# Performance work log

Hardware: AMD Instinct MI355X
Metric: run time of the kernel (lower is better)

## Reference

```python
import jax, jax.numpy as jnp
import numpy as np

B, T, D = 2, 2048, 1024
F = 4096
E = 8


def setup_inputs() -> dict:
    key = jax.random.key(0)
    k0, k1, k2, k3 = jax.random.split(key, 4)
    x = jax.random.normal(k0, (B, T, D), dtype=jnp.float32)
    Wg = jax.random.normal(k1, (E, D), dtype=jnp.float32) * 0.02   # gate Linear weight [E, D]
    W1 = jax.random.normal(k2, (E, D, F), dtype=jnp.float32) * 0.02  # expert up-proj
    W2 = jax.random.normal(k3, (E, F, D), dtype=jnp.float32) * 0.02  # expert down-proj
    return {"x": x, "Wg": Wg, "W1": W1, "W2": W2}


def reference(x, Wg, W1, W2):
    b, t, d = x.shape
    h = x.reshape(-1, d)                              # [N, D], N = b*t
    # --- top-2 gate ---
    logits = h @ Wg.T                                 # [N, E]
    scores, idx = jax.lax.top_k(logits, 2)            # [N, 2], [N, 2]
    scores = jax.nn.softmax(scores.astype(jnp.float32), axis=-1).astype(x.dtype)
    # --- all-expert dense FFN (SiLU MLP) ---
    up = jnp.einsum('nd,edf->enf', h, W1)             # [E, N, F]
    act = jax.nn.silu(up)
    out = jnp.einsum('enf,efd->ned', act, W2)         # [N, E, D]
    # --- combine top-2 ---
    sel = jnp.take_along_axis(out, idx[:, :, None], axis=1)  # [N, 2, D]
    y = jnp.sum(scores[:, :, None] * sel, axis=1)     # [N, D]
    return y.reshape(b, t, d)
```

## Files before the change

### kernel.cpp

```cpp
#include <hip/hip_runtime.h>
#include <hip/hip_bf16.h>
#include <stdint.h>

#define N_TOK 4096
#define D_DIM 1024
#define F_DIM 4096
#define E_NUM 8

typedef unsigned short u16;
typedef __attribute__((ext_vector_type(8))) short short8;
typedef __attribute__((ext_vector_type(4))) float f32x4;

__device__ __forceinline__ u16 f2bf(float f) {
  union { float f; uint32_t u; } v; v.f = f;
  uint32_t u = v.u;
  uint32_t r = (u + 0x7FFFu + ((u >> 16) & 1u)) >> 16;
  return (u16)r;
}

__device__ __forceinline__ void gld_lds16(const u16* g, u16* l) {
  __builtin_amdgcn_global_load_lds(
      (const __attribute__((address_space(1))) uint32_t*)g,
      (__attribute__((address_space(3))) uint32_t*)l, 16, 0, 0);
}

__global__ __launch_bounds__(256) void transpose_cvt_kernel(
    const float* __restrict__ in, u16* __restrict__ out, int R, int C) {
  __shared__ u16 tile[64][72];
  int e = blockIdx.z;
  int r0 = blockIdx.y * 64, c0 = blockIdx.x * 64;
  const float* src = in + (size_t)e * R * C;
  u16* dst = out + (size_t)e * R * C;
  int tid = threadIdx.x;
  int lr = tid & 15;
  int rr = tid >> 4;
#pragma unroll
  for (int p = 0; p < 4; ++p) {
    int r = rr + p * 16;
    float4 v = *(const float4*)&src[(size_t)(r0 + r) * C + c0 + lr * 4];
    tile[lr * 4 + 0][r] = f2bf(v.x);
    tile[lr * 4 + 1][r] = f2bf(v.y);
    tile[lr * 4 + 2][r] = f2bf(v.z);
    tile[lr * 4 + 3][r] = f2bf(v.w);
  }
  __syncthreads();
#pragma unroll
  for (int p = 0; p < 4; ++p) {
    int c = rr + p * 16;
    ushort4 o = *(const ushort4*)&tile[c][lr * 4];
    *(ushort4*)&dst[(size_t)(c0 + c) * R + r0 + lr * 4] = o;
  }
}

__global__ void gate_kernel(const float* __restrict__ x, const float* __restrict__ Wg,
                            u16* __restrict__ xb, int2* __restrict__ choice,
                            float* __restrict__ sc2) {
  int n = blockIdx.x;
  int l = threadIdx.x;
  const float* xr = x + (size_t)n * D_DIM;
  u16* xbr = xb + (size_t)n * D_DIM;
  float acc[E_NUM];
#pragma unroll
  for (int e = 0; e < E_NUM; ++e) acc[e] = 0.f;
  for (int d = l; d < D_DIM; d += 64) {
    float xv = xr[d];
    xbr[d] = f2bf(xv);
#pragma unroll
    for (int e = 0; e < E_NUM; ++e) acc[e] += xv * Wg[e * D_DIM + d];
  }
#pragma unroll
  for (int e = 0; e < E_NUM; ++e) {
    float v = acc[e];
#pragma unroll
    for (int off = 32; off > 0; off >>= 1) v += __shfl_xor(v, off);
    acc[e] = v;
  }
  if (l == 0) {
    int i0 = 0; float m0 = acc[0];
#pragma unroll
    for (int e = 1; e < E_NUM; ++e) if (acc[e] > m0) { m0 = acc[e]; i0 = e; }
    int i1 = -1; float m1 = -INFINITY;
#pragma unroll
    for (int e = 0; e < E_NUM; ++e) if (e != i0 && acc[e] > m1) { m1 = acc[e]; i1 = e; }
    float z = __expf(m1 - m0);
    float s0 = 1.f / (1.f + z);
    sc2[n * 2 + 0] = s0;
    sc2[n * 2 + 1] = 1.f - s0;
    choice[n] = make_int2(i0, i1);
  }
}

__global__ void route_kernel(const int2* __restrict__ choice, int* __restrict__ cnt,
                             int* __restrict__ tok_list) {
  int e = blockIdx.x;
  int l = threadIdx.x;
  unsigned long long below = (l == 0) ? 0ull : ((~0ull) >> (64 - l));
  int c = 0;
  for (int it = 0; it < N_TOK / 64; ++it) {
    int n = it * 64 + l;
    int2 ch = choice[n];
    unsigned long long b0 = __ballot(ch.x == e);
    if (ch.x == e) tok_list[e * N_TOK + c + __popcll(b0 & below)] = 2 * n;
    c += __popcll(b0);
    unsigned long long b1 = __ballot(ch.y == e);
    if (ch.y == e) tok_list[e * N_TOK + c + __popcll(b1 & below)] = 2 * n + 1;
    c += __popcll(b1);
  }
  if (l == 0) cnt[e] = c;
}

__global__ void prefix_kernel(const int* __restrict__ cnt, int* __restrict__ base) {
  if (threadIdx.x == 0) {
    int s = 0;
    for (int e = 0; e < E_NUM; ++e) { base[e] = s; s += cnt[e]; }
  }
}


__global__ __launch_bounds__(256) void up_gemm(
    const u16* __restrict__ xb, const u16* __restrict__ w1t,
    const int* __restrict__ cnt, const int* __restrict__ base,
    const int* __restrict__ tok_list, u16* __restrict__ act) {
  __shared__ u16 As[128 * 32];
  __shared__ u16 Bs[128 * 32];

  const int bid = blockIdx.x;
  const int orig = (bid & 7) * 1024 + (bid >> 3);
  const int bx = orig & 31, by = (orig >> 5) & 31, e = orig >> 10;

  const int ce = cnt[e];
  const int row0 = by * 128;
  if (row0 >= ce) return;
  const int col0 = bx * 128;
  const int be = base[e];

  const int tid = threadIdx.x;
  const int wave = tid >> 6, lane = tid & 63;
  const int wm = wave >> 1, wn = wave & 1;
  const int lr = lane & 15, kq = lane >> 4;

  const int rs0 = wave * 32 + (lane >> 2);
  const int rs1 = rs0 + 16;
  const int kb = (((lane & 3) ^ ((lane >> 3) & 3)) * 8);
  const int kq8 = ((kq ^ ((lr >> 1) & 3)) * 8);

  int ga0 = row0 + rs0, ga1 = row0 + rs1;
  int e0 = (ga0 < ce) ? (tok_list[e * N_TOK + ga0] & (2 * N_TOK - 1)) : 0;
  int e1 = (ga1 < ce) ? (tok_list[e * N_TOK + ga1] & (2 * N_TOK - 1)) : 0;
  const u16* srcA0 = xb + (e0 >> 1) * D_DIM + kb;
  const u16* srcA1 = xb + (e1 >> 1) * D_DIM + kb;
  const u16* srcB0 = w1t + (size_t)(e * F_DIM + col0 + rs0) * D_DIM + kb;
  const u16* srcB1 = w1t + (size_t)(e * F_DIM + col0 + rs1) * D_DIM + kb;
  u16* ldsA0 = As + (wave * 2 + 0) * 512;
  u16* ldsA1 = As + (wave * 2 + 1) * 512;
  u16* ldsB0 = Bs + (wave * 2 + 0) * 512;
  u16* ldsB1 = Bs + (wave * 2 + 1) * 512;

  f32x4 acc[4][4];
#pragma unroll
  for (int m = 0; m < 4; ++m)
#pragma unroll
    for (int n = 0; n < 4; ++n) acc[m][n] = (f32x4){0.f, 0.f, 0.f, 0.f};

  for (int k0 = 0; k0 < D_DIM; k0 += 32) {
    gld_lds16(srcA0 + k0, ldsA0);
    gld_lds16(srcA1 + k0, ldsA1);
    gld_lds16(srcB0 + k0, ldsB0);
    gld_lds16(srcB1 + k0, ldsB1);
    __syncthreads();
    short8 a[4], b[4];
#pragma unroll
    for (int m = 0; m < 4; ++m)
      a[m] = *(const short8*)&As[(wm * 64 + m * 16 + lr) * 32 + kq8];
#pragma unroll
    for (int n = 0; n < 4; ++n)
      b[n] = *(const short8*)&Bs[(wn * 64 + n * 16 + lr) * 32 + kq8];
#pragma unroll
    for (int m = 0; m < 4; ++m)
#pragma unroll
      for (int n = 0; n < 4; ++n)
        acc[m][n] = __builtin_amdgcn_mfma_f32_16x16x32_bf16(a[m], b[n], acc[m][n], 0, 0, 0);
    __syncthreads();
  }

#pragma unroll
  for (int m = 0; m < 4; ++m) {
#pragma unroll
    for (int rg = 0; rg < 4; ++rg) {
      int row = wm * 64 + m * 16 + kq * 4 + rg;
      int i = row0 + row;
      if (i < ce) {
        u16* dst = act + (size_t)(be + i) * F_DIM + col0 + wn * 64;
#pragma unroll
        for (int n = 0; n < 4; ++n) {
          float v = acc[m][n][rg];
          float s = v / (1.f + __expf(-v));
          dst[n * 16 + lr] = f2bf(s);
        }
      }
    }
  }
}

__global__ __launch_bounds__(512) void down_gemm(
    const u16* __restrict__ act, const u16* __restrict__ w2t,
    const int* __restrict__ cnt, const int* __restrict__ base,
    const int* __restrict__ tok_list, const float* __restrict__ sc2,
    float* __restrict__ out) {
  __shared__ u16 As[2][128 * 32];
  __shared__ u16 Bs[2][128 * 32];
  __shared__ int toks[128];

  const int bid = blockIdx.x;
  const int orig = (bid & 7) * 256 + (bid >> 3);
  const int bx = orig & 7, by = (orig >> 3) & 31, e = orig >> 8;

  const int ce = cnt[e];
  const int row0 = by * 128;
  if (row0 >= ce) return;
  const int col0 = bx * 128;
  const int be = base[e];

  const int tid = threadIdx.x;
  const int wave = tid >> 6, lane = tid & 63;
  const int wm = wave >> 2, wn = wave & 3;
  const int lr = lane & 15, kq = lane >> 4;

  if (tid < 128) {
    int i = row0 + tid;
    toks[tid] = (i < ce) ? tok_list[e * N_TOK + i] : -1;
  }
  __syncthreads();

  const int rsA = wave * 16 + (lane >> 2);
  const int kb = (((lane & 3) ^ ((lane >> 3) & 3)) * 8);
  const int kq8 = ((kq ^ ((lr >> 1) & 3)) * 8);

  int ra = min(be + row0 + rsA, 2 * N_TOK - 1);
  const u16* srcA = act + (size_t)ra * F_DIM + kb;
  const u16* srcB = w2t + (size_t)(e * D_DIM + col0 + rsA) * F_DIM + kb;

  f32x4 acc[4][2];
#pragma unroll
  for (int m = 0; m < 4; ++m)
#pragma unroll
    for (int n = 0; n < 2; ++n) acc[m][n] = (f32x4){0.f, 0.f, 0.f, 0.f};

#define DSTAGE(k0, b)                              \
  do {                                             \
    gld_lds16(srcA + (k0), &As[b][wave * 512]);    \
    gld_lds16(srcB + (k0), &Bs[b][wave * 512]);    \
  } while (0)

#define DCOMPUTE(b)                                                           \
  do {                                                                        \
    short8 a[4], bb[2];                                                       \
    _Pragma("unroll") for (int m = 0; m < 4; ++m)                             \
        a[m] = *(const short8*)&As[b][(wm * 64 + m * 16 + lr) * 32 + kq8];    \
    _Pragma("unroll") for (int n = 0; n < 2; ++n)                             \
        bb[n] = *(const short8*)&Bs[b][(wn * 32 + n * 16 + lr) * 32 + kq8];   \
    _Pragma("unroll") for (int m = 0; m < 4; ++m)                             \
        _Pragma("unroll") for (int n = 0; n < 2; ++n)                         \
            acc[m][n] = __builtin_amdgcn_mfma_f32_16x16x32_bf16(a[m], bb[n], acc[m][n], 0, 0, 0); \
  } while (0)

  const int NT = F_DIM / 32;
  DSTAGE(0, 0);
  DSTAGE(32, 1);
  asm volatile("s_waitcnt vmcnt(2)" ::: "memory");
  __builtin_amdgcn_s_barrier();
  __builtin_amdgcn_sched_barrier(0);
  int cur = 0;
  for (int t = 0; t < NT; ++t) {
    DCOMPUTE(cur);
    __builtin_amdgcn_sched_barrier(0);
    __builtin_amdgcn_s_barrier();
    __builtin_amdgcn_sched_barrier(0);
    if (t + 2 < NT) {
      DSTAGE((t + 2) * 32, cur);
      asm volatile("s_waitcnt vmcnt(2)" ::: "memory");
    } else {
      asm volatile("s_waitcnt vmcnt(0)" ::: "memory");
    }
    __builtin_amdgcn_s_barrier();
    __builtin_amdgcn_sched_barrier(0);
    cur ^= 1;
  }
#undef DSTAGE
#undef DCOMPUTE

#pragma unroll
  for (int m = 0; m < 4; ++m) {
#pragma unroll
    for (int rg = 0; rg < 4; ++rg) {
      int row = wm * 64 + m * 16 + kq * 4 + rg;
      int ent = toks[row];
      if (ent >= 0) {
        int tokn = ent >> 1;
        float sc = sc2[tokn * 2 + (ent & 1)];
        float* dst = out + (size_t)tokn * D_DIM + col0 + wn * 32;
#pragma unroll
        for (int n = 0; n < 2; ++n)
          atomicAdd(&dst[n * 16 + lr], acc[m][n][rg] * sc);
      }
    }
  }
}

extern "C" void kernel_launch(void* const* d_in, const int* in_sizes, int n_in,
                              void* d_out, int out_size, void* d_ws, size_t ws_size,
                              hipStream_t stream) {
  const float* x  = (const float*)d_in[0];
  const float* Wg = (const float*)d_in[1];
  const float* W1 = (const float*)d_in[2];
  const float* W2 = (const float*)d_in[3];
  float* out = (float*)d_out;

  char* ws = (char*)d_ws;
  size_t off = 0;
  u16* xb  = (u16*)(ws + off); off += (size_t)N_TOK * D_DIM * 2;
  u16* w1t = (u16*)(ws + off); off += (size_t)E_NUM * F_DIM * D_DIM * 2;
  u16* w2t = (u16*)(ws + off); off += (size_t)E_NUM * D_DIM * F_DIM * 2;
  u16* act = (u16*)(ws + off); off += (size_t)2 * N_TOK * F_DIM * 2;
  int* tok_list = (int*)(ws + off); off += (size_t)E_NUM * N_TOK * 4;
  float* sc2 = (float*)(ws + off); off += (size_t)N_TOK * 2 * 4;
  int2* choice = (int2*)(ws + off); off += (size_t)N_TOK * 8;
  int* cnt  = (int*)(ws + off); off += 128;
  int* base = (int*)(ws + off); off += 128;

  hipMemsetAsync(d_out, 0, (size_t)out_size * 4, stream);

  {
    dim3 blk(256, 1, 1);
    dim3 g1(F_DIM / 64, D_DIM / 64, E_NUM);
    transpose_cvt_kernel<<<g1, blk, 0, stream>>>(W1, w1t, D_DIM, F_DIM);
    dim3 g2(D_DIM / 64, F_DIM / 64, E_NUM);
    transpose_cvt_kernel<<<g2, blk, 0, stream>>>(W2, w2t, F_DIM, D_DIM);
  }

  gate_kernel<<<N_TOK, 64, 0, stream>>>(x, Wg, xb, choice, sc2);
  route_kernel<<<E_NUM, 64, 0, stream>>>(choice, cnt, tok_list);
  prefix_kernel<<<1, 1, 0, stream>>>(cnt, base);

  up_gemm<<<dim3(8192), 256, 0, stream>>>(xb, w1t, cnt, base, tok_list, act);
  down_gemm<<<dim3(2048), 512, 0, stream>>>(act, w2t, cnt, base, tok_list, sc2, out);
}
```

Baseline: 327.2 us.

## Enlarge down-proj GEMM tile to 256x128 with K=64 stages

```diff
diff --git a/kernel.cpp b/kernel.cpp
--- a/kernel.cpp
+++ b/kernel.cpp
@@ -116,7 +116,6 @@
   }
 }
 
-
 __global__ __launch_bounds__(256) void up_gemm(
     const u16* __restrict__ xb, const u16* __restrict__ w1t,
     const int* __restrict__ cnt, const int* __restrict__ base,
@@ -207,67 +206,81 @@
     const int* __restrict__ cnt, const int* __restrict__ base,
     const int* __restrict__ tok_list, const float* __restrict__ sc2,
     float* __restrict__ out) {
-  __shared__ u16 As[2][128 * 32];
-  __shared__ u16 Bs[2][128 * 32];
-  __shared__ int toks[128];
+  __shared__ u16 As[2][256 * 64];
+  __shared__ u16 Bs[2][128 * 64];
+  __shared__ int toks[256];
 
   const int bid = blockIdx.x;
-  const int orig = (bid & 7) * 256 + (bid >> 3);
-  const int bx = orig & 7, by = (orig >> 3) & 31, e = orig >> 8;
+  const int orig = (bid & 7) * 128 + (bid >> 3);
+  const int bx = orig & 7, by = (orig >> 3) & 15, e = orig >> 7;
 
   const int ce = cnt[e];
-  const int row0 = by * 128;
+  const int row0 = by * 256;
   if (row0 >= ce) return;
   const int col0 = bx * 128;
   const int be = base[e];
 
   const int tid = threadIdx.x;
   const int wave = tid >> 6, lane = tid & 63;
-  const int wm = wave >> 2, wn = wave & 3;
+  const int wm = wave >> 1, wn = wave & 1;
   const int lr = lane & 15, kq = lane >> 4;
 
-  if (tid < 128) {
+  if (tid < 256) {
     int i = row0 + tid;
     toks[tid] = (i < ce) ? tok_list[e * N_TOK + i] : -1;
   }
   __syncthreads();
 
-  const int rsA = wave * 16 + (lane >> 2);
-  const int kb = (((lane & 3) ^ ((lane >> 3) & 3)) * 8);
-  const int kq8 = ((kq ^ ((lr >> 1) & 3)) * 8);
-
-  int ra = min(be + row0 + rsA, 2 * N_TOK - 1);
-  const u16* srcA = act + (size_t)ra * F_DIM + kb;
-  const u16* srcB = w2t + (size_t)(e * D_DIM + col0 + rsA) * F_DIM + kb;
-
-  f32x4 acc[4][2];
+  const int srow = lane >> 3;
+  const int kb = ((lane & 7) ^ srow) * 8;
+  const int rsw = (lr & 7);
+
+  const u16* srcA[4];
+#pragma unroll
+  for (int j = 0; j < 4; ++j) {
+    int ra = min(be + row0 + wave * 32 + j * 8 + srow, 2 * N_TOK - 1);
+    srcA[j] = act + (size_t)ra * F_DIM + kb;
+  }
+  const u16* srcB[2];
+#pragma unroll
+  for (int j = 0; j < 2; ++j) {
+    int rb = e * D_DIM + col0 + wave * 16 + j * 8 + srow;
+    srcB[j] = w2t + (size_t)rb * F_DIM + kb;
+  }
+
+  f32x4 acc[4][4];
 #pragma unroll
   for (int m = 0; m < 4; ++m)
 #pragma unroll
-    for (int n = 0; n < 2; ++n) acc[m][n] = (f32x4){0.f, 0.f, 0.f, 0.f};
-
-#define DSTAGE(k0, b)                              \
-  do {                                             \
-    gld_lds16(srcA + (k0), &As[b][wave * 512]);    \
-    gld_lds16(srcB + (k0), &Bs[b][wave * 512]);    \
+    for (int n = 0; n < 4; ++n) acc[m][n] = (f32x4){0.f, 0.f, 0.f, 0.f};
+
+#define DSTAGE(k0, b)                                              \
+  do {                                                             \
+    _Pragma("unroll") for (int j = 0; j < 4; ++j)                  \
+        gld_lds16(srcA[j] + (k0), &As[b][(wave * 4 + j) * 512]);   \
+    _Pragma("unroll") for (int j = 0; j < 2; ++j)                  \
+        gld_lds16(srcB[j] + (k0), &Bs[b][(wave * 2 + j) * 512]);   \
   } while (0)
 
-#define DCOMPUTE(b)                                                           \
-  do {                                                                        \
-    short8 a[4], bb[2];                                                       \
-    _Pragma("unroll") for (int m = 0; m < 4; ++m)                             \
-        a[m] = *(const short8*)&As[b][(wm * 64 + m * 16 + lr) * 32 + kq8];    \
-    _Pragma("unroll") for (int n = 0; n < 2; ++n)                             \
-        bb[n] = *(const short8*)&Bs[b][(wn * 32 + n * 16 + lr) * 32 + kq8];   \
-    _Pragma("unroll") for (int m = 0; m < 4; ++m)                             \
-        _Pragma("unroll") for (int n = 0; n < 2; ++n)                         \
-            acc[m][n] = __builtin_amdgcn_mfma_f32_16x16x32_bf16(a[m], bb[n], acc[m][n], 0, 0, 0); \
+#define DCOMPUTE(b)                                                             \
+  do {                                                                          \
+    _Pragma("unroll") for (int kk = 0; kk < 2; ++kk) {                          \
+      const int ks = ((kk * 4 + kq) ^ rsw) * 8;                                 \
+      short8 a[4], bb[4];                                                       \
+      _Pragma("unroll") for (int m = 0; m < 4; ++m)                             \
+          a[m] = *(const short8*)&As[b][(wm * 64 + m * 16 + lr) * 64 + ks];     \
+      _Pragma("unroll") for (int n = 0; n < 4; ++n)                             \
+          bb[n] = *(const short8*)&Bs[b][(wn * 64 + n * 16 + lr) * 64 + ks];    \
+      _Pragma("unroll") for (int m = 0; m < 4; ++m)                             \
+          _Pragma("unroll") for (int n = 0; n < 4; ++n)                         \
+              acc[m][n] = __builtin_amdgcn_mfma_f32_16x16x32_bf16(a[m], bb[n], acc[m][n], 0, 0, 0); \
+    }                                                                           \
   } while (0)
 
-  const int NT = F_DIM / 32;
+  const int NT = F_DIM / 64;
   DSTAGE(0, 0);
-  DSTAGE(32, 1);
-  asm volatile("s_waitcnt vmcnt(2)" ::: "memory");
+  DSTAGE(64, 1);
+  asm volatile("s_waitcnt vmcnt(6)" ::: "memory");
   __builtin_amdgcn_s_barrier();
   __builtin_amdgcn_sched_barrier(0);
   int cur = 0;
@@ -277,8 +290,8 @@
     __builtin_amdgcn_s_barrier();
     __builtin_amdgcn_sched_barrier(0);
     if (t + 2 < NT) {
-      DSTAGE((t + 2) * 32, cur);
-      asm volatile("s_waitcnt vmcnt(2)" ::: "memory");
+      DSTAGE((t + 2) * 64, cur);
+      asm volatile("s_waitcnt vmcnt(6)" ::: "memory");
     } else {
       asm volatile("s_waitcnt vmcnt(0)" ::: "memory");
     }
@@ -298,9 +311,9 @@
       if (ent >= 0) {
         int tokn = ent >> 1;
         float sc = sc2[tokn * 2 + (ent & 1)];
-        float* dst = out + (size_t)tokn * D_DIM + col0 + wn * 32;
-#pragma unroll
-        for (int n = 0; n < 2; ++n)
+        float* dst = out + (size_t)tokn * D_DIM + col0 + wn * 64;
+#pragma unroll
+        for (int n = 0; n < 4; ++n)
           atomicAdd(&dst[n * 16 + lr], acc[m][n][rg] * sc);
       }
     }
@@ -343,5 +356,5 @@
   prefix_kernel<<<1, 1, 0, stream>>>(cnt, base);
 
   up_gemm<<<dim3(8192), 256, 0, stream>>>(xb, w1t, cnt, base, tok_list, act);
-  down_gemm<<<dim3(2048), 512, 0, stream>>>(act, w2t, cnt, base, tok_list, sc2, out);
-}
+  down_gemm<<<dim3(1024), 512, 0, stream>>>(act, w2t, cnt, base, tok_list, sc2, out);
+}
```

New measurement: 399.8 us. +22.2%, slower.

## Double-buffer up_gemm LDS tiles and widen block to eight waves

Applied to the files above, without the earlier changes.

```diff
diff --git a/kernel.cpp b/kernel.cpp
--- a/kernel.cpp
+++ b/kernel.cpp
@@ -116,13 +116,12 @@
   }
 }
 
-
-__global__ __launch_bounds__(256) void up_gemm(
+__global__ __launch_bounds__(512) void up_gemm(
     const u16* __restrict__ xb, const u16* __restrict__ w1t,
     const int* __restrict__ cnt, const int* __restrict__ base,
     const int* __restrict__ tok_list, u16* __restrict__ act) {
-  __shared__ u16 As[128 * 32];
-  __shared__ u16 Bs[128 * 32];
+  __shared__ u16 As[2][128 * 32];
+  __shared__ u16 Bs[2][128 * 32];
 
   const int bid = blockIdx.x;
   const int orig = (bid & 7) * 1024 + (bid >> 3);
@@ -136,52 +135,66 @@
 
   const int tid = threadIdx.x;
   const int wave = tid >> 6, lane = tid & 63;
-  const int wm = wave >> 1, wn = wave & 1;
+  const int wm = wave >> 2, wn = wave & 3;
   const int lr = lane & 15, kq = lane >> 4;
 
-  const int rs0 = wave * 32 + (lane >> 2);
-  const int rs1 = rs0 + 16;
+  const int rsA = wave * 16 + (lane >> 2);
   const int kb = (((lane & 3) ^ ((lane >> 3) & 3)) * 8);
   const int kq8 = ((kq ^ ((lr >> 1) & 3)) * 8);
 
-  int ga0 = row0 + rs0, ga1 = row0 + rs1;
-  int e0 = (ga0 < ce) ? (tok_list[e * N_TOK + ga0] & (2 * N_TOK - 1)) : 0;
-  int e1 = (ga1 < ce) ? (tok_list[e * N_TOK + ga1] & (2 * N_TOK - 1)) : 0;
-  const u16* srcA0 = xb + (e0 >> 1) * D_DIM + kb;
-  const u16* srcA1 = xb + (e1 >> 1) * D_DIM + kb;
-  const u16* srcB0 = w1t + (size_t)(e * F_DIM + col0 + rs0) * D_DIM + kb;
-  const u16* srcB1 = w1t + (size_t)(e * F_DIM + col0 + rs1) * D_DIM + kb;
-  u16* ldsA0 = As + (wave * 2 + 0) * 512;
-  u16* ldsA1 = As + (wave * 2 + 1) * 512;
-  u16* ldsB0 = Bs + (wave * 2 + 0) * 512;
-  u16* ldsB1 = Bs + (wave * 2 + 1) * 512;
-
-  f32x4 acc[4][4];
+  int ga = row0 + rsA;
+  int e0 = (ga < ce) ? (tok_list[e * N_TOK + ga] & (2 * N_TOK - 1)) : 0;
+  const u16* srcA = xb + (e0 >> 1) * D_DIM + kb;
+  const u16* srcB = w1t + (size_t)(e * F_DIM + col0 + rsA) * D_DIM + kb;
+
+  f32x4 acc[4][2];
 #pragma unroll
   for (int m = 0; m < 4; ++m)
 #pragma unroll
-    for (int n = 0; n < 4; ++n) acc[m][n] = (f32x4){0.f, 0.f, 0.f, 0.f};
-
-  for (int k0 = 0; k0 < D_DIM; k0 += 32) {
-    gld_lds16(srcA0 + k0, ldsA0);
-    gld_lds16(srcA1 + k0, ldsA1);
-    gld_lds16(srcB0 + k0, ldsB0);
-    gld_lds16(srcB1 + k0, ldsB1);
-    __syncthreads();
-    short8 a[4], b[4];
-#pragma unroll
-    for (int m = 0; m < 4; ++m)
-      a[m] = *(const short8*)&As[(wm * 64 + m * 16 + lr) * 32 + kq8];
-#pragma unroll
-    for (int n = 0; n < 4; ++n)
-      b[n] = *(const short8*)&Bs[(wn * 64 + n * 16 + lr) * 32 + kq8];
-#pragma unroll
-    for (int m = 0; m < 4; ++m)
-#pragma unroll
-      for (int n = 0; n < 4; ++n)
-        acc[m][n] = __builtin_amdgcn_mfma_f32_16x16x32_bf16(a[m], b[n], acc[m][n], 0, 0, 0);
-    __syncthreads();
-  }
+    for (int n = 0; n < 2; ++n) acc[m][n] = (f32x4){0.f, 0.f, 0.f, 0.f};
+
+#define USTAGE(k0, b)                              \
+  do {                                             \
+    gld_lds16(srcA + (k0), &As[b][wave * 512]);    \
+    gld_lds16(srcB + (k0), &Bs[b][wave * 512]);    \
+  } while (0)
+
+#define UCOMPUTE(b)                                                           \
+  do {                                                                        \
+    short8 a[4], bb[2];                                                       \
+    _Pragma("unroll") for (int m = 0; m < 4; ++m)                             \
+        a[m] = *(const short8*)&As[b][(wm * 64 + m * 16 + lr) * 32 + kq8];    \
+    _Pragma("unroll") for (int n = 0; n < 2; ++n)                             \
+        bb[n] = *(const short8*)&Bs[b][(wn * 32 + n * 16 + lr) * 32 + kq8];   \
+    _Pragma("unroll") for (int m = 0; m < 4; ++m)                             \
+        _Pragma("unroll") for (int n = 0; n < 2; ++n)                         \
+            acc[m][n] = __builtin_amdgcn_mfma_f32_16x16x32_bf16(a[m], bb[n], acc[m][n], 0, 0, 0); \
+  } while (0)
+
+  const int NT = D_DIM / 32;
+  USTAGE(0, 0);
+  USTAGE(32, 1);
+  asm volatile("s_waitcnt vmcnt(2)" ::: "memory");
+  __builtin_amdgcn_s_barrier();
+  __builtin_amdgcn_sched_barrier(0);
+  int cur = 0;
+  for (int t = 0; t < NT; ++t) {
+    UCOMPUTE(cur);
+    __builtin_amdgcn_sched_barrier(0);
+    __builtin_amdgcn_s_barrier();
+    __builtin_amdgcn_sched_barrier(0);
+    if (t + 2 < NT) {
+      USTAGE((t + 2) * 32, cur);
+      asm volatile("s_waitcnt vmcnt(2)" ::: "memory");
+    } else {
+      asm volatile("s_waitcnt vmcnt(0)" ::: "memory");
+    }
+    __builtin_amdgcn_s_barrier();
+    __builtin_amdgcn_sched_barrier(0);
+    cur ^= 1;
+  }
+#undef USTAGE
+#undef UCOMPUTE
 
 #pragma unroll
   for (int m = 0; m < 4; ++m) {
@@ -190,9 +203,9 @@
       int row = wm * 64 + m * 16 + kq * 4 + rg;
       int i = row0 + row;
       if (i < ce) {
-        u16* dst = act + (size_t)(be + i) * F_DIM + col0 + wn * 64;
-#pragma unroll
-        for (int n = 0; n < 4; ++n) {
+        u16* dst = act + (size_t)(be + i) * F_DIM + col0 + wn * 32;
+#pragma unroll
+        for (int n = 0; n < 2; ++n) {
           float v = acc[m][n][rg];
           float s = v / (1.f + __expf(-v));
           dst[n * 16 + lr] = f2bf(s);
@@ -342,6 +355,6 @@
   route_kernel<<<E_NUM, 64, 0, stream>>>(choice, cnt, tok_list);
   prefix_kernel<<<1, 1, 0, stream>>>(cnt, base);
 
-  up_gemm<<<dim3(8192), 256, 0, stream>>>(xb, w1t, cnt, base, tok_list, act);
+  up_gemm<<<dim3(8192), 512, 0, stream>>>(xb, w1t, cnt, base, tok_list, act);
   down_gemm<<<dim3(2048), 512, 0, stream>>>(act, w2t, cnt, base, tok_list, sc2, out);
 }
```

After: 326.7 us. Within noise of the previous version (-0.1%).
